# Kernel optimization log

Hardware: AMD Instinct MI355X
Metric: run time of the kernel (lower is better)

The kernel has to match this reference:

```python
import jax, jax.numpy as jnp
import numpy as np

N, C, H, W, HD = 32, 24, 12, 12, 128
GT, FP, A = 256, 256, 28
DIN = (C + 2) * 2 + HD  # 180, g_theta input dim


def setup_inputs() -> dict:
    key = jax.random.key(0)
    ks = jax.random.split(key, 18)
    def w(k, shape):
        fan_in = shape[0]
        return jax.random.normal(k, shape, jnp.float32) / np.sqrt(fan_in).astype(np.float32)
    inp = {
        "x": jax.random.normal(ks[0], (N, C, H, W), jnp.float32),
        "q": jax.random.normal(ks[1], (N, HD), jnp.float32),
        "gW0": w(ks[2], (DIN, GT)), "gb0": jnp.zeros((GT,), jnp.float32),
        "gW1": w(ks[3], (GT, GT)),  "gb1": jnp.zeros((GT,), jnp.float32),
        "gW2": w(ks[4], (GT, GT)),  "gb2": jnp.zeros((GT,), jnp.float32),
        "gW3": w(ks[5], (GT, GT)),  "gb3": jnp.zeros((GT,), jnp.float32),
        "fW0": w(ks[6], (GT, FP)),  "fb0": jnp.zeros((FP,), jnp.float32),
        "fW1": w(ks[7], (FP, FP)),  "fb1": jnp.zeros((FP,), jnp.float32),
        "fW2": w(ks[8], (FP, A)),   "fb2": jnp.zeros((A,), jnp.float32),
    }
    return inp


def _rn_forward(x, q, gW0, gb0, gW1, gb1, gW2, gb2, gW3, gb3,
                fW0, fb0, fW1, fb1, fW2, fb2):
    n, c, h, w = x.shape
    o = h * w
    # rn_encode: per-object features + (x, y) coordinates in [-1, 1]
    feats = x.reshape(n, c, o).transpose(0, 2, 1)            # [n, o, c]
    xc = jnp.repeat(jnp.linspace(-1.0, 1.0, h), w)           # row coord per pixel
    yc = jnp.tile(jnp.linspace(-1.0, 1.0, w), h)             # col coord per pixel
    coords = jnp.stack([xc, yc], axis=-1).astype(x.dtype)    # [o, 2]
    feats = jnp.concatenate([feats, jnp.broadcast_to(coords, (n, o, 2))], axis=-1)  # [n, o, c+2]
    cp = c + 2
    # pairs[n, a, b] = [feats[b], feats[a], q]  (matches torch unsqueeze(1)/unsqueeze(2))
    pairs = jnp.concatenate([
        jnp.broadcast_to(feats[:, None, :, :], (n, o, o, cp)),
        jnp.broadcast_to(feats[:, :, None, :], (n, o, o, cp)),
        jnp.broadcast_to(q[:, None, None, :], (n, o, o, q.shape[1])),
    ], axis=-1)                                              # [n, o, o, 2*cp+hd]
    # g_theta: 4-layer ReLU MLP applied per pair
    hdd = pairs
    for Wm, b in ((gW0, gb0), (gW1, gb1), (gW2, gb2), (gW3, gb3)):
        hdd = jax.nn.relu(jnp.einsum('nabd,de->nabe', hdd, Wm) + b)
    # lower_sum: keep lower-triangular (incl. diagonal) pairs, sum over them
    mask = jnp.tril(jnp.ones((o, o), hdd.dtype))[None, :, :, None]
    rel = jnp.sum(hdd * mask, axis=(1, 2))                   # [n, GT]
    # f_phi: ReLU hidden layers, linear output (dropout = eval mode no-op)
    y = jax.nn.relu(rel @ fW0 + fb0)
    y = jax.nn.relu(y @ fW1 + fb1)
    logits = y @ fW2 + fb2                                   # [n, A]
    return logits


def reference(x, q, gW0, gb0, gW1, gb1, gW2, gb2, gW3, gb3,
              fW0, fb0, fW1, fb1, fW2, fb2):
    return _rn_forward(x, q, gW0, gb0, gW1, gb1, gW2, gb2, gW3, gb3,
                       fW0, fb0, fW1, fb1, fW2, fb2)
```

## Files before the change

### kernel.cpp

```cpp
#include <hip/hip_runtime.h>
#include <hip/hip_bf16.h>

typedef __attribute__((ext_vector_type(8))) short short8;
typedef __attribute__((ext_vector_type(4))) float f32x4;

#define O 144
#define NB 32
#define GT 256
#define NPAIRS 10440
#define TP 128
#define NT 82

#define WS_WT   0u
#define WS_U    393216u
#define WS_V    2752512u
#define WS_REL  5144576u

__device__ __forceinline__ unsigned short f2bf(float f){
  unsigned int uu = __builtin_bit_cast(unsigned int, f);
  unsigned int lsb = (uu >> 16) & 1u;
  uu += 0x7fffu + lsb;
  return (unsigned short)(uu >> 16);
}
__device__ __forceinline__ unsigned int cvtpk(float lo, float hi){
  unsigned int r;
  asm("v_cvt_pk_bf16_f32 %0, %1, %2" : "=v"(r) : "v"(lo), "v"(hi));
  return r;
}

__global__ void prep_uv(const float* __restrict__ x, const float* __restrict__ q,
                        const float* __restrict__ gW0, const float* __restrict__ gb0,
                        unsigned short* __restrict__ u, unsigned short* __restrict__ v){
  __shared__ float xs[24][18];
  __shared__ float qs[128];
  int n = blockIdx.x >> 3, oq = blockIdx.x & 7;
  int t = threadIdx.x;
  int o0 = oq * 18;
  for (int i = t; i < 432; i += 256){
    int c = i / 18, oo = i - c*18;
    xs[c][oo] = x[(n*24 + c)*144 + o0 + oo];
  }
  if (t < 128) qs[t] = q[n*128 + t];
  __syncthreads();
  float wq = gb0[t];
  for (int d = 0; d < 128; d++) wq += qs[d] * gW0[(52 + d)*GT + t];
  float wc[52];
  #pragma unroll
  for (int c = 0; c < 52; c++) wc[c] = gW0[c*GT + t];
  for (int oo = 0; oo < 18; oo++){
    int o = o0 + oo;
    float xc = -1.f + 2.f * (float)(o / 12) / 11.f;
    float yc = -1.f + 2.f * (float)(o % 12) / 11.f;
    float su = wq + xc*wc[24] + yc*wc[25];
    float sv =      xc*wc[50] + yc*wc[51];
    #pragma unroll
    for (int c = 0; c < 24; c++){ float f = xs[c][oo]; su += f*wc[c]; sv += f*wc[26+c]; }
    u[(size_t)(n*O + o)*GT + t] = f2bf(su);
    v[(size_t)(n*O + o)*GT + t] = f2bf(sv);
  }
}

__global__ void prep_wt(const float* __restrict__ gW1, const float* __restrict__ gW2,
                        const float* __restrict__ gW3, unsigned short* __restrict__ WtP,
                        float* __restrict__ rel){
  int li = blockIdx.x >> 8;
  int e  = blockIdx.x & 255;
  int k  = threadIdx.x;
  const float* W = (li == 0) ? gW1 : (li == 1) ? gW2 : gW3;
  int et = e >> 4, r = e & 15;
  int kk = k >> 5, g = (k >> 3) & 3, d = k & 7;
  WtP[li*65536 + et*4096 + kk*512 + r*32 + g*8 + d] = f2bf(W[k*GT + e]);
  if (blockIdx.x < NB) rel[blockIdx.x*GT + k] = 0.f;
}

__global__ __launch_bounds__(256, 2) void rn_main(
    const unsigned short* __restrict__ u, const unsigned short* __restrict__ v,
    const unsigned short* __restrict__ WtP,
    const float* __restrict__ gb1, const float* __restrict__ gb2,
    const float* __restrict__ gb3, float* __restrict__ rel)
{
  __shared__ short8 hbuf[4096];
  char* lds = (char*)hbuf;

  const int tid  = threadIdx.x;
  const int lane = tid & 63;
  const int wav  = tid >> 6;
  const int n    = blockIdx.x / NT;
  const int tile = blockIdx.x - n*NT;
  const int tbase = tile * TP;
  const int l15 = lane & 15, l4 = lane >> 4;

  const unsigned short* wbase = WtP + wav*16384 + l15*32 + l4*8;
  short8 an0, an1, an2, an3;
#define LOADA(p_) { const unsigned short* _wp = wbase + ((p_) >> 3)*65536 + ((p_) & 7)*512; \
    an0 = *(const short8*)(_wp);         an1 = *(const short8*)(_wp + 4096);               \
    an2 = *(const short8*)(_wp + 8192);  an3 = *(const short8*)(_wp + 12288); }
  LOADA(0);

  {
    int row = wav*32 + (lane >> 1);
    int pt  = tbase + row;
    bool valid = pt < NPAIRS;
    int pa = 0, pb = 0;
    if (valid){
      pa = (int)((sqrtf(8.f*(float)pt + 1.f) - 1.f) * 0.5f);
      while ((pa + 1)*(pa + 2)/2 <= pt) pa++;
      while (pa*(pa + 1)/2 > pt) pa--;
      pb = pt - pa*(pa + 1)/2;
    }
    const uint4* up4 = (const uint4*)(u + (size_t)(n*O + pb)*GT);
    const uint4* vp4 = (const uint4*)(v + (size_t)(n*O + pa)*GT);
    int half = lane & 1;
    int sbase = row*512 + half*256;
    int ts = ((lane >> 1) & 7) << 4;
    #pragma unroll
    for (int cc = 0; cc < 16; cc++){
      uint4 hv;
      if (valid){
        uint4 uu = up4[half*16 + cc];
        uint4 vv = vp4[half*16 + cc];
        #pragma unroll
        for (int j = 0; j < 4; j++){
          unsigned int ud = (&uu.x)[j], vd = (&vv.x)[j];
          float lo = __builtin_bit_cast(float, ud << 16) + __builtin_bit_cast(float, vd << 16);
          float hi = __builtin_bit_cast(float, ud & 0xffff0000u) + __builtin_bit_cast(float, vd & 0xffff0000u);
          (&hv.x)[j] = cvtpk(fmaxf(lo, 0.f), fmaxf(hi, 0.f));
        }
      } else {
        hv = (uint4){0u, 0u, 0u, 0u};
      }
      *(uint4*)(lds + sbase + ((cc*16) ^ ts)) = hv;
    }
  }
  __syncthreads();

  const bool fullvalid = (tbase + TP <= NPAIRS);
  const int swz01 = (l15 & 3) << 4;
  const int swz2  = (l15 & 4) << 4;
  const int rbE = l15*512 + ((l4*16) ^ swz01) + swz2;
  const int rbO = l15*512 + ((l4*16) ^ swz01) - swz2;
  const int ebase = l15*512 + wav*128 + ((l4*8) ^ ((l15 & 1) << 4)) + ((l15 & 6) << 4);
  f32x4 acc[4][8];

  #pragma unroll
  for (int L = 0; L < 3; L++){
    const float* gb = (L == 0) ? gb1 : (L == 1) ? gb2 : gb3;

    #pragma unroll
    for (int ie = 0; ie < 4; ie++){
      f32x4 bbv = *(const f32x4*)(gb + wav*64 + ie*16 + l4*4);
      #pragma unroll
      for (int jp = 0; jp < 8; jp++) acc[ie][jp] = bbv;
    }

    #pragma unroll
    for (int kk = 0; kk < 8; kk++){
      short8 a0 = an0, a1 = an1, a2 = an2, a3 = an3;
      int pn = L*8 + kk + 1; if (pn > 23) pn = 23;
      LOADA(pn);
      const int rb = (kk & 1) ? rbO : rbE;
      short8 b[8];
      #pragma unroll
      for (int jp = 0; jp < 8; jp++)
        b[jp] = *(short8*)(lds + rb + jp*8192 + kk*64);
      __builtin_amdgcn_s_setprio(1);
      #pragma unroll
      for (int jp = 0; jp < 8; jp++){
        acc[0][jp] = __builtin_amdgcn_mfma_f32_16x16x32_bf16(a0, b[jp], acc[0][jp], 0, 0, 0);
        acc[1][jp] = __builtin_amdgcn_mfma_f32_16x16x32_bf16(a1, b[jp], acc[1][jp], 0, 0, 0);
        acc[2][jp] = __builtin_amdgcn_mfma_f32_16x16x32_bf16(a2, b[jp], acc[2][jp], 0, 0, 0);
        acc[3][jp] = __builtin_amdgcn_mfma_f32_16x16x32_bf16(a3, b[jp], acc[3][jp], 0, 0, 0);
      }
      __builtin_amdgcn_s_setprio(0);
    }

    if (L < 2){
      __syncthreads();
      #pragma unroll
      for (int ie = 0; ie < 4; ie++){
        int ea = ebase ^ (ie*32);
        #pragma unroll
        for (int jp = 0; jp < 8; jp++){
          uint2 pk;
          pk.x = cvtpk(fmaxf(acc[ie][jp][0], 0.f), fmaxf(acc[ie][jp][1], 0.f));
          pk.y = cvtpk(fmaxf(acc[ie][jp][2], 0.f), fmaxf(acc[ie][jp][3], 0.f));
          *(uint2*)(lds + ea + jp*8192) = pk;
        }
      }
      __syncthreads();
    } else {
      #pragma unroll
      for (int ie = 0; ie < 4; ie++){
        int e0 = wav*64 + ie*16 + l4*4;
        f32x4 s = {0.f, 0.f, 0.f, 0.f};
        #pragma unroll
        for (int jp = 0; jp < 8; jp++){
          bool pv = fullvalid || (tbase + jp*16 + l15 < NPAIRS);
          #pragma unroll
          for (int j = 0; j < 4; j++){
            float hvv = fmaxf(acc[ie][jp][j], 0.f);
            s[j] += pv ? hvv : 0.f;
          }
        }
        #pragma unroll
        for (int st = 1; st < 16; st <<= 1){
          #pragma unroll
          for (int j = 0; j < 4; j++)
            s[j] += __shfl_xor(s[j], st);
        }
        if (l15 == 0){
          #pragma unroll
          for (int j = 0; j < 4; j++)
            atomicAdd(&rel[n*GT + e0 + j], s[j]);
        }
      }
    }
  }
#undef LOADA
}

__global__ void fphi(const float* __restrict__ rel,
                     const float* __restrict__ fW0, const float* __restrict__ fb0,
                     const float* __restrict__ fW1, const float* __restrict__ fb1,
                     const float* __restrict__ fW2, const float* __restrict__ fb2,
                     float* __restrict__ out){
  int n = blockIdx.x, t = threadIdx.x;
  __shared__ float h[256], y[256];
  h[t] = rel[n*GT + t];
  __syncthreads();
  float s = fb0[t];
  for (int k = 0; k < 256; k++) s += h[k] * fW0[k*GT + t];
  y[t] = fmaxf(s, 0.f);
  __syncthreads();
  s = fb1[t];
  for (int k = 0; k < 256; k++) s += y[k] * fW1[k*GT + t];
  __syncthreads();
  h[t] = fmaxf(s, 0.f);
  __syncthreads();
  if (t < 28){
    s = fb2[t];
    for (int k = 0; k < 256; k++) s += h[k] * fW2[k*28 + t];
    out[n*28 + t] = s;
  }
}

extern "C" void kernel_launch(void* const* d_in, const int* in_sizes, int n_in,
                              void* d_out, int out_size, void* d_ws, size_t ws_size,
                              hipStream_t stream){
  (void)in_sizes; (void)n_in; (void)out_size; (void)ws_size;
  const float* x   = (const float*)d_in[0];
  const float* q   = (const float*)d_in[1];
  const float* gW0 = (const float*)d_in[2];
  const float* gb0 = (const float*)d_in[3];
  const float* gW1 = (const float*)d_in[4];
  const float* gb1 = (const float*)d_in[5];
  const float* gW2 = (const float*)d_in[6];
  const float* gb2 = (const float*)d_in[7];
  const float* gW3 = (const float*)d_in[8];
  const float* gb3 = (const float*)d_in[9];
  const float* fW0 = (const float*)d_in[10];
  const float* fb0 = (const float*)d_in[11];
  const float* fW1 = (const float*)d_in[12];
  const float* fb1 = (const float*)d_in[13];
  const float* fW2 = (const float*)d_in[14];
  const float* fb2 = (const float*)d_in[15];

  char* ws = (char*)d_ws;
  unsigned short* WtP = (unsigned short*)(ws + WS_WT);
  unsigned short* u   = (unsigned short*)(ws + WS_U);
  unsigned short* v   = (unsigned short*)(ws + WS_V);
  float* rel = (float*)(ws + WS_REL);
  float* out = (float*)d_out;

  hipLaunchKernelGGL(prep_uv, dim3(NB*8), dim3(256), 0, stream, x, q, gW0, gb0, u, v);
  hipLaunchKernelGGL(prep_wt, dim3(768),  dim3(256), 0, stream, gW1, gW2, gW3, WtP, rel);
  hipLaunchKernelGGL(rn_main, dim3(NB*NT), dim3(256), 0, stream,
                     u, v, WtP, gb1, gb2, gb3, rel);
  hipLaunchKernelGGL(fphi, dim3(NB), dim3(256), 0, stream,
                     rel, fW0, fb0, fW1, fb1, fW2, fb2, out);
}
```

Before: 255.7 us.

## Switch to 32x32 MFMA, double-buffer LDS reads, fuse prep and f_phi kernels

The main MLP loop moves from 16x16x32 to 32x32x16 bf16 MFMA tiles, with a new weight packing, new LDS swizzles and double-buffered B-operand loads. The two prep kernels merge into one launch, and f_phi is folded into rn_main's tail: the last block finishing each batch, detected with an atomic counter, runs it. Block indices are also remapped to spread batches across XCDs. This removes two launches and aims for higher MFMA throughput per LDS read, at the cost of more accumulator registers and a serialized tail block.

New measurement: 392.3 us. +53.4%, slower.

```diff
diff --git a/kernel.cpp b/kernel.cpp
--- a/kernel.cpp
+++ b/kernel.cpp
@@ -3,6 +3,7 @@
 
 typedef __attribute__((ext_vector_type(8))) short short8;
 typedef __attribute__((ext_vector_type(4))) float f32x4;
+typedef __attribute__((ext_vector_type(16))) float f32x16;
 
 #define O 144
 #define NB 32
@@ -10,11 +11,13 @@
 #define NPAIRS 10440
 #define TP 128
 #define NT 82
+#define GRID (NB*NT)
 
 #define WS_WT   0u
 #define WS_U    393216u
 #define WS_V    2752512u
 #define WS_REL  5144576u
+#define WS_CNT  5177344u
 
 __device__ __forceinline__ unsigned short f2bf(float f){
   unsigned int uu = __builtin_bit_cast(unsigned int, f);
@@ -28,56 +31,62 @@
   return r;
 }
 
-__global__ void prep_uv(const float* __restrict__ x, const float* __restrict__ q,
-                        const float* __restrict__ gW0, const float* __restrict__ gb0,
-                        unsigned short* __restrict__ u, unsigned short* __restrict__ v){
-  __shared__ float xs[24][18];
-  __shared__ float qs[128];
-  int n = blockIdx.x >> 3, oq = blockIdx.x & 7;
-  int t = threadIdx.x;
-  int o0 = oq * 18;
-  for (int i = t; i < 432; i += 256){
-    int c = i / 18, oo = i - c*18;
-    xs[c][oo] = x[(n*24 + c)*144 + o0 + oo];
+__global__ void prep_all(const float* __restrict__ x, const float* __restrict__ q,
+                         const float* __restrict__ gW0, const float* __restrict__ gb0,
+                         const float* __restrict__ gW1, const float* __restrict__ gW2,
+                         const float* __restrict__ gW3,
+                         unsigned short* __restrict__ u, unsigned short* __restrict__ v,
+                         unsigned short* __restrict__ WtP, float* __restrict__ rel,
+                         int* __restrict__ cnt){
+  int blk = blockIdx.x, t = threadIdx.x;
+  if (blk < 256){
+    __shared__ float xs[24][18];
+    __shared__ float qs[128];
+    int n = blk >> 3, oq = blk & 7;
+    int o0 = oq * 18;
+    for (int i = t; i < 432; i += 256){
+      int c = i / 18, oo = i - c*18;
+      xs[c][oo] = x[(n*24 + c)*144 + o0 + oo];
+    }
+    if (t < 128) qs[t] = q[n*128 + t];
+    __syncthreads();
+    float wq = gb0[t];
+    for (int d = 0; d < 128; d++) wq += qs[d] * gW0[(52 + d)*GT + t];
+    float wc[52];
+    #pragma unroll
+    for (int c = 0; c < 52; c++) wc[c] = gW0[c*GT + t];
+    for (int oo = 0; oo < 18; oo++){
+      int o = o0 + oo;
+      float xc = -1.f + 2.f * (float)(o / 12) / 11.f;
+      float yc = -1.f + 2.f * (float)(o % 12) / 11.f;
+      float su = wq + xc*wc[24] + yc*wc[25];
+      float sv =      xc*wc[50] + yc*wc[51];
+      #pragma unroll
+      for (int c = 0; c < 24; c++){ float f = xs[c][oo]; su += f*wc[c]; sv += f*wc[26+c]; }
+      u[(size_t)(n*O + o)*GT + t] = f2bf(su);
+      v[(size_t)(n*O + o)*GT + t] = f2bf(sv);
+    }
+  } else {
+    int b2 = blk - 256;
+    int li = b2 >> 8, e = b2 & 255;
+    int k = t;
+    const float* W = (li == 0) ? gW1 : (li == 1) ? gW2 : gW3;
+    WtP[li*65536 + (e>>5)*8192 + (k>>4)*512 + (e&31)*16 + ((k>>3)&1)*8 + (k&7)]
+        = f2bf(W[k*GT + e]);
+    if (b2 < NB) rel[b2*GT + t] = 0.f;
+    if (b2 == 0 && t < NB) cnt[t] = 0;
   }
-  if (t < 128) qs[t] = q[n*128 + t];
-  __syncthreads();
-  float wq = gb0[t];
-  for (int d = 0; d < 128; d++) wq += qs[d] * gW0[(52 + d)*GT + t];
-  float wc[52];
-  #pragma unroll
-  for (int c = 0; c < 52; c++) wc[c] = gW0[c*GT + t];
-  for (int oo = 0; oo < 18; oo++){
-    int o = o0 + oo;
-    float xc = -1.f + 2.f * (float)(o / 12) / 11.f;
-    float yc = -1.f + 2.f * (float)(o % 12) / 11.f;
-    float su = wq + xc*wc[24] + yc*wc[25];
-    float sv =      xc*wc[50] + yc*wc[51];
-    #pragma unroll
-    for (int c = 0; c < 24; c++){ float f = xs[c][oo]; su += f*wc[c]; sv += f*wc[26+c]; }
-    u[(size_t)(n*O + o)*GT + t] = f2bf(su);
-    v[(size_t)(n*O + o)*GT + t] = f2bf(sv);
-  }
-}
-
-__global__ void prep_wt(const float* __restrict__ gW1, const float* __restrict__ gW2,
-                        const float* __restrict__ gW3, unsigned short* __restrict__ WtP,
-                        float* __restrict__ rel){
-  int li = blockIdx.x >> 8;
-  int e  = blockIdx.x & 255;
-  int k  = threadIdx.x;
-  const float* W = (li == 0) ? gW1 : (li == 1) ? gW2 : gW3;
-  int et = e >> 4, r = e & 15;
-  int kk = k >> 5, g = (k >> 3) & 3, d = k & 7;
-  WtP[li*65536 + et*4096 + kk*512 + r*32 + g*8 + d] = f2bf(W[k*GT + e]);
-  if (blockIdx.x < NB) rel[blockIdx.x*GT + k] = 0.f;
 }
 
 __global__ __launch_bounds__(256, 2) void rn_main(
     const unsigned short* __restrict__ u, const unsigned short* __restrict__ v,
     const unsigned short* __restrict__ WtP,
     const float* __restrict__ gb1, const float* __restrict__ gb2,
-    const float* __restrict__ gb3, float* __restrict__ rel)
+    const float* __restrict__ gb3, float* __restrict__ rel, int* __restrict__ cnt,
+    const float* __restrict__ fW0, const float* __restrict__ fb0,
+    const float* __restrict__ fW1, const float* __restrict__ fb1,
+    const float* __restrict__ fW2, const float* __restrict__ fb2,
+    float* __restrict__ out)
 {
   __shared__ short8 hbuf[4096];
   char* lds = (char*)hbuf;
@@ -85,16 +94,16 @@
   const int tid  = threadIdx.x;
   const int lane = tid & 63;
   const int wav  = tid >> 6;
-  const int n    = blockIdx.x / NT;
-  const int tile = blockIdx.x - n*NT;
+  int lg = (blockIdx.x & 7)*328 + (blockIdx.x >> 3);
+  const int n    = lg / NT;
+  const int tile = lg - n*NT;
   const int tbase = tile * TP;
-  const int l15 = lane & 15, l4 = lane >> 4;
-
-  const unsigned short* wbase = WtP + wav*16384 + l15*32 + l4*8;
-  short8 an0, an1, an2, an3;
-#define LOADA(p_) { const unsigned short* _wp = wbase + ((p_) >> 3)*65536 + ((p_) & 7)*512; \
-    an0 = *(const short8*)(_wp);         an1 = *(const short8*)(_wp + 4096);               \
-    an2 = *(const short8*)(_wp + 8192);  an3 = *(const short8*)(_wp + 12288); }
+  const int l31 = lane & 31, l32 = lane >> 5;
+
+  const unsigned short* wb = WtP + wav*16384 + l31*16 + l32*8;
+  short8 a0n, a1n;
+#define LOADA(p_) { const unsigned short* _wp = wb + ((p_) >> 4)*65536 + ((p_) & 15)*512; \
+    a0n = *(const short8*)(_wp); a1n = *(const short8*)(_wp + 8192); }
   LOADA(0);
 
   {
@@ -135,41 +144,62 @@
   __syncthreads();
 
   const bool fullvalid = (tbase + TP <= NPAIRS);
-  const int swz01 = (l15 & 3) << 4;
-  const int swz2  = (l15 & 4) << 4;
-  const int rbE = l15*512 + ((l4*16) ^ swz01) + swz2;
-  const int rbO = l15*512 + ((l4*16) ^ swz01) - swz2;
-  const int ebase = l15*512 + wav*128 + ((l4*8) ^ ((l15 & 1) << 4)) + ((l15 & 6) << 4);
-  f32x4 acc[4][8];
+  const int l13 = (lane >> 1) & 3;
+  const int l03 = lane & 3;
+  const int l2b = (lane >> 2) & 1;
+  int rb[4];
+  #pragma unroll
+  for (int m = 0; m < 4; m++)
+    rb[m] = l31*512 + ((m ^ l13) << 5) + ((l32 << 4) ^ ((lane & 1) << 4));
+  const int eb = l31*512 + l32*8 + wav*128;
+
+  f32x16 acc[2][4];
+  short8 b0[4], b1[4];
+#define LOADB(dst_, ks_) { \
+    dst_[0] = *(short8*)(lds + rb[(ks_) & 3] + (((ks_) >> 2)*128)); \
+    dst_[1] = *(short8*)(lds + rb[(ks_) & 3] + (((ks_) >> 2)*128 + 16384)); \
+    dst_[2] = *(short8*)(lds + rb[(ks_) & 3] + (((ks_) >> 2)*128 + 32768)); \
+    dst_[3] = *(short8*)(lds + rb[(ks_) & 3] + (((ks_) >> 2)*128 + 49152)); }
 
   #pragma unroll
   for (int L = 0; L < 3; L++){
     const float* gb = (L == 0) ? gb1 : (L == 1) ? gb2 : gb3;
 
     #pragma unroll
-    for (int ie = 0; ie < 4; ie++){
-      f32x4 bbv = *(const f32x4*)(gb + wav*64 + ie*16 + l4*4);
+    for (int et = 0; et < 2; et++){
       #pragma unroll
-      for (int jp = 0; jp < 8; jp++) acc[ie][jp] = bbv;
-    }
-
+      for (int qq = 0; qq < 4; qq++){
+        f32x4 bb = *(const f32x4*)(gb + wav*64 + et*32 + qq*8 + l32*4);
+        #pragma unroll
+        for (int rr = 0; rr < 4; rr++){
+          #pragma unroll
+          for (int jp = 0; jp < 4; jp++) acc[et][jp][qq*4 + rr] = bb[rr];
+        }
+      }
+    }
+
+    LOADB(b0, 0);
     #pragma unroll
-    for (int kk = 0; kk < 8; kk++){
-      short8 a0 = an0, a1 = an1, a2 = an2, a3 = an3;
-      int pn = L*8 + kk + 1; if (pn > 23) pn = 23;
+    for (int ks = 0; ks < 16; ks++){
+      short8 a0 = a0n, a1 = a1n;
+      int pn = L*16 + ks + 1; if (pn > 47) pn = 47;
       LOADA(pn);
-      const int rb = (kk & 1) ? rbO : rbE;
-      short8 b[8];
-      #pragma unroll
-      for (int jp = 0; jp < 8; jp++)
-        b[jp] = *(short8*)(lds + rb + jp*8192 + kk*64);
+      if (ks < 15){
+        if (ks & 1) { LOADB(b0, ks + 1); } else { LOADB(b1, ks + 1); }
+      }
       __builtin_amdgcn_s_setprio(1);
-      #pragma unroll
-      for (int jp = 0; jp < 8; jp++){
-        acc[0][jp] = __builtin_amdgcn_mfma_f32_16x16x32_bf16(a0, b[jp], acc[0][jp], 0, 0, 0);
-        acc[1][jp] = __builtin_amdgcn_mfma_f32_16x16x32_bf16(a1, b[jp], acc[1][jp], 0, 0, 0);
-        acc[2][jp] = __builtin_amdgcn_mfma_f32_16x16x32_bf16(a2, b[jp], acc[2][jp], 0, 0, 0);
-        acc[3][jp] = __builtin_amdgcn_mfma_f32_16x16x32_bf16(a3, b[jp], acc[3][jp], 0, 0, 0);
+      if ((ks & 1) == 0){
+        #pragma unroll
+        for (int jp = 0; jp < 4; jp++){
+          acc[0][jp] = __builtin_amdgcn_mfma_f32_32x32x16_bf16(a0, b0[jp], acc[0][jp], 0, 0, 0);
+          acc[1][jp] = __builtin_amdgcn_mfma_f32_32x32x16_bf16(a1, b0[jp], acc[1][jp], 0, 0, 0);
+        }
+      } else {
+        #pragma unroll
+        for (int jp = 0; jp < 4; jp++){
+          acc[0][jp] = __builtin_amdgcn_mfma_f32_32x32x16_bf16(a0, b1[jp], acc[0][jp], 0, 0, 0);
+          acc[1][jp] = __builtin_amdgcn_mfma_f32_32x32x16_bf16(a1, b1[jp], acc[1][jp], 0, 0, 0);
+        }
       }
       __builtin_amdgcn_s_setprio(0);
     }
@@ -177,70 +207,81 @@
     if (L < 2){
       __syncthreads();
       #pragma unroll
-      for (int ie = 0; ie < 4; ie++){
-        int ea = ebase ^ (ie*32);
-        #pragma unroll
-        for (int jp = 0; jp < 8; jp++){
-          uint2 pk;
-          pk.x = cvtpk(fmaxf(acc[ie][jp][0], 0.f), fmaxf(acc[ie][jp][1], 0.f));
-          pk.y = cvtpk(fmaxf(acc[ie][jp][2], 0.f), fmaxf(acc[ie][jp][3], 0.f));
-          *(uint2*)(lds + ea + jp*8192) = pk;
+      for (int et = 0; et < 2; et++){
+        #pragma unroll
+        for (int qq = 0; qq < 4; qq++){
+          int ea = eb + (((qq ^ l03) << 4) | ((et ^ l2b) << 6));
+          #pragma unroll
+          for (int jp = 0; jp < 4; jp++){
+            uint2 w;
+            w.x = cvtpk(fmaxf(acc[et][jp][qq*4+0], 0.f), fmaxf(acc[et][jp][qq*4+1], 0.f));
+            w.y = cvtpk(fmaxf(acc[et][jp][qq*4+2], 0.f), fmaxf(acc[et][jp][qq*4+3], 0.f));
+            *(uint2*)(lds + ea + jp*16384) = w;
+          }
         }
       }
       __syncthreads();
     } else {
       #pragma unroll
-      for (int ie = 0; ie < 4; ie++){
-        int e0 = wav*64 + ie*16 + l4*4;
-        f32x4 s = {0.f, 0.f, 0.f, 0.f};
-        #pragma unroll
-        for (int jp = 0; jp < 8; jp++){
-          bool pv = fullvalid || (tbase + jp*16 + l15 < NPAIRS);
-          #pragma unroll
-          for (int j = 0; j < 4; j++){
-            float hvv = fmaxf(acc[ie][jp][j], 0.f);
-            s[j] += pv ? hvv : 0.f;
+      for (int et = 0; et < 2; et++){
+        f32x16 s;
+        #pragma unroll
+        for (int r = 0; r < 16; r++) s[r] = 0.f;
+        #pragma unroll
+        for (int jp = 0; jp < 4; jp++){
+          bool pv = fullvalid || (tbase + jp*32 + l31 < NPAIRS);
+          #pragma unroll
+          for (int r = 0; r < 16; r++){
+            float hv = fmaxf(acc[et][jp][r], 0.f);
+            s[r] += pv ? hv : 0.f;
           }
         }
         #pragma unroll
-        for (int st = 1; st < 16; st <<= 1){
-          #pragma unroll
-          for (int j = 0; j < 4; j++)
-            s[j] += __shfl_xor(s[j], st);
-        }
-        if (l15 == 0){
-          #pragma unroll
-          for (int j = 0; j < 4; j++)
-            atomicAdd(&rel[n*GT + e0 + j], s[j]);
+        for (int st = 1; st < 32; st <<= 1){
+          #pragma unroll
+          for (int r = 0; r < 16; r++)
+            s[r] += __shfl_xor(s[r], st);
+        }
+        if (l31 == 0){
+          #pragma unroll
+          for (int r = 0; r < 16; r++)
+            atomicAdd(&rel[n*GT + wav*64 + et*32 + (r&3) + 8*(r>>2) + 4*l32], s[r]);
         }
       }
     }
   }
 #undef LOADA
-}
-
-__global__ void fphi(const float* __restrict__ rel,
-                     const float* __restrict__ fW0, const float* __restrict__ fb0,
-                     const float* __restrict__ fW1, const float* __restrict__ fb1,
-                     const float* __restrict__ fW2, const float* __restrict__ fb2,
-                     float* __restrict__ out){
-  int n = blockIdx.x, t = threadIdx.x;
-  __shared__ float h[256], y[256];
-  h[t] = rel[n*GT + t];
+#undef LOADB
+
+  __threadfence();
   __syncthreads();
-  float s = fb0[t];
-  for (int k = 0; k < 256; k++) s += h[k] * fW0[k*GT + t];
-  y[t] = fmaxf(s, 0.f);
+  if (tid == 0) ((int*)lds)[0] = atomicAdd(&cnt[n], 1);
   __syncthreads();
-  s = fb1[t];
-  for (int k = 0; k < 256; k++) s += y[k] * fW1[k*GT + t];
+  int done = ((int*)lds)[0];
   __syncthreads();
-  h[t] = fmaxf(s, 0.f);
-  __syncthreads();
-  if (t < 28){
-    s = fb2[t];
-    for (int k = 0; k < 256; k++) s += h[k] * fW2[k*28 + t];
-    out[n*28 + t] = s;
+  if (done == NT - 1){
+    __threadfence();
+    float* hsm = (float*)lds;
+    float* ysm = hsm + 256;
+    int t = tid;
+    float rv = atomicAdd(&rel[n*GT + t], 0.f);
+    __syncthreads();
+    hsm[t] = rv;
+    __syncthreads();
+    float s = fb0[t];
+    for (int k = 0; k < 256; k++) s += hsm[k] * fW0[k*GT + t];
+    ysm[t] = fmaxf(s, 0.f);
+    __syncthreads();
+    s = fb1[t];
+    for (int k = 0; k < 256; k++) s += ysm[k] * fW1[k*GT + t];
+    __syncthreads();
+    hsm[t] = fmaxf(s, 0.f);
+    __syncthreads();
+    if (t < 28){
+      s = fb2[t];
+      for (int k = 0; k < 256; k++) s += hsm[k] * fW2[k*28 + t];
+      out[n*28 + t] = s;
+    }
   }
 }
 
@@ -270,12 +311,12 @@
   unsigned short* u   = (unsigned short*)(ws + WS_U);
   unsigned short* v   = (unsigned short*)(ws + WS_V);
   float* rel = (float*)(ws + WS_REL);
+  int*   cnt = (int*)(ws + WS_CNT);
   float* out = (float*)d_out;
 
-  hipLaunchKernelGGL(prep_uv, dim3(NB*8), dim3(256), 0, stream, x, q, gW0, gb0, u, v);
-  hipLaunchKernelGGL(prep_wt, dim3(768),  dim3(256), 0, stream, gW1, gW2, gW3, WtP, rel);
-  hipLaunchKernelGGL(rn_main, dim3(NB*NT), dim3(256), 0, stream,
-                     u, v, WtP, gb1, gb2, gb3, rel);
-  hipLaunchKernelGGL(fphi, dim3(NB), dim3(256), 0, stream,
-                     rel, fW0, fb0, fW1, fb1, fW2, fb2, out);
-}
+  hipLaunchKernelGGL(prep_all, dim3(1024), dim3(256), 0, stream,
+                     x, q, gW0, gb0, gW1, gW2, gW3, u, v, WtP, rel, cnt);
+  hipLaunchKernelGGL(rn_main, dim3(GRID), dim3(256), 0, stream,
+                     u, v, WtP, gb1, gb2, gb3, rel, cnt,
+                     fW0, fb0, fW1, fb1, fW2, fb2, out);
+}
```

## Fuse prep kernels and f_phi tail, shrink pair tile, deepen weight prefetch

Applied to the files above, without the earlier changes.

Merges the two prep kernels into one launch and folds the f_phi MLP into the main kernel through a per-batch completion counter, so the last block for each batch runs the head. The pair tile shrinks from 128 to 96 (grid of 109 tiles per batch) and block indices are remapped across XCD-style groups of 8. Weight fragments are now prefetched three k-steps ahead in rotating register sets instead of one. This removes two launches and may improve load balance and hide global-load latency, at the cost of more registers and a serialized tail on the last block of each batch. The counter-based tail also relies on the atomic rel reads seeing every other block's adds.

Result: faster. 241.7 us (-5.5%).

```diff
diff --git a/kernel.cpp b/kernel.cpp
--- a/kernel.cpp
+++ b/kernel.cpp
@@ -8,13 +8,16 @@
 #define NB 32
 #define GT 256
 #define NPAIRS 10440
-#define TP 128
-#define NT 82
+#define TP 96
+#define NT 109
+#define GRID (NB*NT)
+#define CHUNK 436
 
 #define WS_WT   0u
 #define WS_U    393216u
 #define WS_V    2752512u
 #define WS_REL  5144576u
+#define WS_CNT  5177344u
 
 __device__ __forceinline__ unsigned short f2bf(float f){
   unsigned int uu = __builtin_bit_cast(unsigned int, f);
@@ -28,77 +31,87 @@
   return r;
 }
 
-__global__ void prep_uv(const float* __restrict__ x, const float* __restrict__ q,
-                        const float* __restrict__ gW0, const float* __restrict__ gb0,
-                        unsigned short* __restrict__ u, unsigned short* __restrict__ v){
-  __shared__ float xs[24][18];
-  __shared__ float qs[128];
-  int n = blockIdx.x >> 3, oq = blockIdx.x & 7;
-  int t = threadIdx.x;
-  int o0 = oq * 18;
-  for (int i = t; i < 432; i += 256){
-    int c = i / 18, oo = i - c*18;
-    xs[c][oo] = x[(n*24 + c)*144 + o0 + oo];
+__global__ void prep_all(const float* __restrict__ x, const float* __restrict__ q,
+                         const float* __restrict__ gW0, const float* __restrict__ gb0,
+                         const float* __restrict__ gW1, const float* __restrict__ gW2,
+                         const float* __restrict__ gW3,
+                         unsigned short* __restrict__ u, unsigned short* __restrict__ v,
+                         unsigned short* __restrict__ WtP, float* __restrict__ rel,
+                         int* __restrict__ cnt){
+  int blk = blockIdx.x, t = threadIdx.x;
+  if (blk < 256){
+    __shared__ float xs[24][18];
+    __shared__ float qs[128];
+    int n = blk >> 3, oq = blk & 7;
+    int o0 = oq * 18;
+    for (int i = t; i < 432; i += 256){
+      int c = i / 18, oo = i - c*18;
+      xs[c][oo] = x[(n*24 + c)*144 + o0 + oo];
+    }
+    if (t < 128) qs[t] = q[n*128 + t];
+    __syncthreads();
+    float wq = gb0[t];
+    for (int d = 0; d < 128; d++) wq += qs[d] * gW0[(52 + d)*GT + t];
+    float wc[52];
+    #pragma unroll
+    for (int c = 0; c < 52; c++) wc[c] = gW0[c*GT + t];
+    for (int oo = 0; oo < 18; oo++){
+      int o = o0 + oo;
+      float xc = -1.f + 2.f * (float)(o / 12) / 11.f;
+      float yc = -1.f + 2.f * (float)(o % 12) / 11.f;
+      float su = wq + xc*wc[24] + yc*wc[25];
+      float sv =      xc*wc[50] + yc*wc[51];
+      #pragma unroll
+      for (int c = 0; c < 24; c++){ float f = xs[c][oo]; su += f*wc[c]; sv += f*wc[26+c]; }
+      u[(size_t)(n*O + o)*GT + t] = f2bf(su);
+      v[(size_t)(n*O + o)*GT + t] = f2bf(sv);
+    }
+  } else {
+    int b2 = blk - 256;
+    int li = b2 >> 8, e = b2 & 255;
+    int k = t;
+    const float* W = (li == 0) ? gW1 : (li == 1) ? gW2 : gW3;
+    int et = e >> 4, r = e & 15;
+    int kk = k >> 5, g = (k >> 3) & 3, d = k & 7;
+    WtP[li*65536 + et*4096 + kk*512 + r*32 + g*8 + d] = f2bf(W[k*GT + e]);
+    if (b2 < NB) rel[b2*GT + t] = 0.f;
+    if (b2 == 0 && t < NB) cnt[t] = 0;
   }
-  if (t < 128) qs[t] = q[n*128 + t];
-  __syncthreads();
-  float wq = gb0[t];
-  for (int d = 0; d < 128; d++) wq += qs[d] * gW0[(52 + d)*GT + t];
-  float wc[52];
-  #pragma unroll
-  for (int c = 0; c < 52; c++) wc[c] = gW0[c*GT + t];
-  for (int oo = 0; oo < 18; oo++){
-    int o = o0 + oo;
-    float xc = -1.f + 2.f * (float)(o / 12) / 11.f;
-    float yc = -1.f + 2.f * (float)(o % 12) / 11.f;
-    float su = wq + xc*wc[24] + yc*wc[25];
-    float sv =      xc*wc[50] + yc*wc[51];
-    #pragma unroll
-    for (int c = 0; c < 24; c++){ float f = xs[c][oo]; su += f*wc[c]; sv += f*wc[26+c]; }
-    u[(size_t)(n*O + o)*GT + t] = f2bf(su);
-    v[(size_t)(n*O + o)*GT + t] = f2bf(sv);
-  }
-}
-
-__global__ void prep_wt(const float* __restrict__ gW1, const float* __restrict__ gW2,
-                        const float* __restrict__ gW3, unsigned short* __restrict__ WtP,
-                        float* __restrict__ rel){
-  int li = blockIdx.x >> 8;
-  int e  = blockIdx.x & 255;
-  int k  = threadIdx.x;
-  const float* W = (li == 0) ? gW1 : (li == 1) ? gW2 : gW3;
-  int et = e >> 4, r = e & 15;
-  int kk = k >> 5, g = (k >> 3) & 3, d = k & 7;
-  WtP[li*65536 + et*4096 + kk*512 + r*32 + g*8 + d] = f2bf(W[k*GT + e]);
-  if (blockIdx.x < NB) rel[blockIdx.x*GT + k] = 0.f;
 }
 
 __global__ __launch_bounds__(256, 2) void rn_main(
     const unsigned short* __restrict__ u, const unsigned short* __restrict__ v,
     const unsigned short* __restrict__ WtP,
     const float* __restrict__ gb1, const float* __restrict__ gb2,
-    const float* __restrict__ gb3, float* __restrict__ rel)
+    const float* __restrict__ gb3, float* __restrict__ rel, int* __restrict__ cnt,
+    const float* __restrict__ fW0, const float* __restrict__ fb0,
+    const float* __restrict__ fW1, const float* __restrict__ fb1,
+    const float* __restrict__ fW2, const float* __restrict__ fb2,
+    float* __restrict__ out)
 {
-  __shared__ short8 hbuf[4096];
+  __shared__ short8 hbuf[3072];
   char* lds = (char*)hbuf;
 
   const int tid  = threadIdx.x;
   const int lane = tid & 63;
   const int wav  = tid >> 6;
-  const int n    = blockIdx.x / NT;
-  const int tile = blockIdx.x - n*NT;
+  int lg = (blockIdx.x & 7)*CHUNK + (blockIdx.x >> 3);
+  const int n    = lg / NT;
+  const int tile = lg - n*NT;
   const int tbase = tile * TP;
   const int l15 = lane & 15, l4 = lane >> 4;
 
-  const unsigned short* wbase = WtP + wav*16384 + l15*32 + l4*8;
-  short8 an0, an1, an2, an3;
-#define LOADA(p_) { const unsigned short* _wp = wbase + ((p_) >> 3)*65536 + ((p_) & 7)*512; \
-    an0 = *(const short8*)(_wp);         an1 = *(const short8*)(_wp + 4096);               \
-    an2 = *(const short8*)(_wp + 8192);  an3 = *(const short8*)(_wp + 12288); }
-  LOADA(0);
-
-  {
-    int row = wav*32 + (lane >> 1);
+  const unsigned short* wb = WtP + wav*16384 + l15*32 + l4*8;
+  short8 aA0,aA1,aA2,aA3, aB0,aB1,aB2,aB3, aC0,aC1,aC2,aC3;
+#define LA(s0,s1,s2,s3,p_) { const unsigned short* _wp = wb + ((p_) >> 3)*65536 + ((p_) & 7)*512; \
+    s0 = *(const short8*)(_wp);        s1 = *(const short8*)(_wp + 4096); \
+    s2 = *(const short8*)(_wp + 8192); s3 = *(const short8*)(_wp + 12288); }
+  LA(aA0,aA1,aA2,aA3, 0)
+  LA(aB0,aB1,aB2,aB3, 1)
+  LA(aC0,aC1,aC2,aC3, 2)
+
+  if (tid < 192){
+    int row = tid >> 1;
     int pt  = tbase + row;
     bool valid = pt < NPAIRS;
     int pa = 0, pb = 0;
@@ -110,9 +123,9 @@
     }
     const uint4* up4 = (const uint4*)(u + (size_t)(n*O + pb)*GT);
     const uint4* vp4 = (const uint4*)(v + (size_t)(n*O + pa)*GT);
-    int half = lane & 1;
+    int half = tid & 1;
     int sbase = row*512 + half*256;
-    int ts = ((lane >> 1) & 7) << 4;
+    int ts = (row & 7) << 4;
     #pragma unroll
     for (int cc = 0; cc < 16; cc++){
       uint4 hv;
@@ -140,7 +153,21 @@
   const int rbE = l15*512 + ((l4*16) ^ swz01) + swz2;
   const int rbO = l15*512 + ((l4*16) ^ swz01) - swz2;
   const int ebase = l15*512 + wav*128 + ((l4*8) ^ ((l15 & 1) << 4)) + ((l15 & 6) << 4);
-  f32x4 acc[4][8];
+  f32x4 acc[4][6];
+
+#define MFMA16(s0,s1,s2,s3,kk_) { \
+    const int rb_ = ((kk_) & 1) ? rbO : rbE; \
+    short8 b_[6]; \
+    _Pragma("unroll") \
+    for (int jp = 0; jp < 6; jp++) b_[jp] = *(short8*)(lds + rb_ + jp*8192 + (kk_)*64); \
+    __builtin_amdgcn_s_setprio(1); \
+    _Pragma("unroll") \
+    for (int jp = 0; jp < 6; jp++){ \
+      acc[0][jp] = __builtin_amdgcn_mfma_f32_16x16x32_bf16(s0, b_[jp], acc[0][jp], 0, 0, 0); \
+      acc[1][jp] = __builtin_amdgcn_mfma_f32_16x16x32_bf16(s1, b_[jp], acc[1][jp], 0, 0, 0); \
+      acc[2][jp] = __builtin_amdgcn_mfma_f32_16x16x32_bf16(s2, b_[jp], acc[2][jp], 0, 0, 0); \
+      acc[3][jp] = __builtin_amdgcn_mfma_f32_16x16x32_bf16(s3, b_[jp], acc[3][jp], 0, 0, 0); } \
+    __builtin_amdgcn_s_setprio(0); }
 
   #pragma unroll
   for (int L = 0; L < 3; L++){
@@ -150,28 +177,16 @@
     for (int ie = 0; ie < 4; ie++){
       f32x4 bbv = *(const f32x4*)(gb + wav*64 + ie*16 + l4*4);
       #pragma unroll
-      for (int jp = 0; jp < 8; jp++) acc[ie][jp] = bbv;
+      for (int jp = 0; jp < 6; jp++) acc[ie][jp] = bbv;
     }
 
     #pragma unroll
     for (int kk = 0; kk < 8; kk++){
-      short8 a0 = an0, a1 = an1, a2 = an2, a3 = an3;
-      int pn = L*8 + kk + 1; if (pn > 23) pn = 23;
-      LOADA(pn);
-      const int rb = (kk & 1) ? rbO : rbE;
-      short8 b[8];
-      #pragma unroll
-      for (int jp = 0; jp < 8; jp++)
-        b[jp] = *(short8*)(lds + rb + jp*8192 + kk*64);
-      __builtin_amdgcn_s_setprio(1);
-      #pragma unroll
-      for (int jp = 0; jp < 8; jp++){
-        acc[0][jp] = __builtin_amdgcn_mfma_f32_16x16x32_bf16(a0, b[jp], acc[0][jp], 0, 0, 0);
-        acc[1][jp] = __builtin_amdgcn_mfma_f32_16x16x32_bf16(a1, b[jp], acc[1][jp], 0, 0, 0);
-        acc[2][jp] = __builtin_amdgcn_mfma_f32_16x16x32_bf16(a2, b[jp], acc[2][jp], 0, 0, 0);
-        acc[3][jp] = __builtin_amdgcn_mfma_f32_16x16x32_bf16(a3, b[jp], acc[3][jp], 0, 0, 0);
-      }
-      __builtin_amdgcn_s_setprio(0);
+      const int p = L*8 + kk;
+      const int pn = (p + 3 > 23) ? 23 : p + 3;
+      if ((p % 3) == 0)      { MFMA16(aA0,aA1,aA2,aA3,kk) LA(aA0,aA1,aA2,aA3,pn) }
+      else if ((p % 3) == 1) { MFMA16(aB0,aB1,aB2,aB3,kk) LA(aB0,aB1,aB2,aB3,pn) }
+      else                   { MFMA16(aC0,aC1,aC2,aC3,kk) LA(aC0,aC1,aC2,aC3,pn) }
     }
 
     if (L < 2){
@@ -180,7 +195,7 @@
       for (int ie = 0; ie < 4; ie++){
         int ea = ebase ^ (ie*32);
         #pragma unroll
-        for (int jp = 0; jp < 8; jp++){
+        for (int jp = 0; jp < 6; jp++){
           uint2 pk;
           pk.x = cvtpk(fmaxf(acc[ie][jp][0], 0.f), fmaxf(acc[ie][jp][1], 0.f));
           pk.y = cvtpk(fmaxf(acc[ie][jp][2], 0.f), fmaxf(acc[ie][jp][3], 0.f));
@@ -194,7 +209,7 @@
         int e0 = wav*64 + ie*16 + l4*4;
         f32x4 s = {0.f, 0.f, 0.f, 0.f};
         #pragma unroll
-        for (int jp = 0; jp < 8; jp++){
+        for (int jp = 0; jp < 6; jp++){
           bool pv = fullvalid || (tbase + jp*16 + l15 < NPAIRS);
           #pragma unroll
           for (int j = 0; j < 4; j++){
@@ -216,31 +231,35 @@
       }
     }
   }
-#undef LOADA
-}
-
-__global__ void fphi(const float* __restrict__ rel,
-                     const float* __restrict__ fW0, const float* __restrict__ fb0,
-                     const float* __restrict__ fW1, const float* __restrict__ fb1,
-                     const float* __restrict__ fW2, const float* __restrict__ fb2,
-                     float* __restrict__ out){
-  int n = blockIdx.x, t = threadIdx.x;
-  __shared__ float h[256], y[256];
-  h[t] = rel[n*GT + t];
+#undef LA
+#undef MFMA16
+
   __syncthreads();
-  float s = fb0[t];
-  for (int k = 0; k < 256; k++) s += h[k] * fW0[k*GT + t];
-  y[t] = fmaxf(s, 0.f);
+  if (tid == 0) ((int*)lds)[0] = atomicAdd(&cnt[n], 1);
   __syncthreads();
-  s = fb1[t];
-  for (int k = 0; k < 256; k++) s += y[k] * fW1[k*GT + t];
+  int done = ((int*)lds)[0];
   __syncthreads();
-  h[t] = fmaxf(s, 0.f);
-  __syncthreads();
-  if (t < 28){
-    s = fb2[t];
-    for (int k = 0; k < 256; k++) s += h[k] * fW2[k*28 + t];
-    out[n*28 + t] = s;
+  if (done == NT - 1){
+    float rv = atomicAdd(&rel[n*GT + tid], 0.f);
+    float* hsm = (float*)lds;
+    float* ysm = hsm + 256;
+    int t = tid;
+    hsm[t] = rv;
+    __syncthreads();
+    float s = fb0[t];
+    for (int k = 0; k < 256; k++) s += hsm[k] * fW0[k*GT + t];
+    ysm[t] = fmaxf(s, 0.f);
+    __syncthreads();
+    s = fb1[t];
+    for (int k = 0; k < 256; k++) s += ysm[k] * fW1[k*GT + t];
+    __syncthreads();
+    hsm[t] = fmaxf(s, 0.f);
+    __syncthreads();
+    if (t < 28){
+      s = fb2[t];
+      for (int k = 0; k < 256; k++) s += hsm[k] * fW2[k*28 + t];
+      out[n*28 + t] = s;
+    }
   }
 }
 
@@ -270,12 +289,12 @@
   unsigned short* u   = (unsigned short*)(ws + WS_U);
   unsigned short* v   = (unsigned short*)(ws + WS_V);
   float* rel = (float*)(ws + WS_REL);
+  int*   cnt = (int*)(ws + WS_CNT);
   float* out = (float*)d_out;
 
-  hipLaunchKernelGGL(prep_uv, dim3(NB*8), dim3(256), 0, stream, x, q, gW0, gb0, u, v);
-  hipLaunchKernelGGL(prep_wt, dim3(768),  dim3(256), 0, stream, gW1, gW2, gW3, WtP, rel);
-  hipLaunchKernelGGL(rn_main, dim3(NB*NT), dim3(256), 0, stream,
-                     u, v, WtP, gb1, gb2, gb3, rel);
-  hipLaunchKernelGGL(fphi, dim3(NB), dim3(256), 0, stream,
-                     rel, fW0, fb0, fW1, fb1, fW2, fb2, out);
-}
+  hipLaunchKernelGGL(prep_all, dim3(1024), dim3(256), 0, stream,
+                     x, q, gW0, gb0, gW1, gW2, gW3, u, v, WtP, rel, cnt);
+  hipLaunchKernelGGL(rn_main, dim3(GRID), dim3(256), 0, stream,
+                     u, v, WtP, gb1, gb2, gb3, rel, cnt,
+                     fW0, fb0, fW1, fb1, fW2, fb2, out);
+}
```
